# Kernel tuning notes

Hardware: AMD Instinct MI355X
Metric: run time of the kernel (lower is better)

Reference implementation:

```python
import jax, jax.numpy as jnp
import numpy as np

B, S, H, M, E = 8, 2048, 2048, 256, 8
Hh = H // 2

def setup_inputs() -> dict:
    key = jax.random.key(0)
    ks = jax.random.split(key, 12)
    s = 0.02
    return {
        "x":   jax.random.normal(ks[0], (B, S, H), dtype=jnp.float32),
        # metacognitive (router) network: H -> M -> M -> E, softmax
        "Wm1": jax.random.normal(ks[1], (H, M), dtype=jnp.float32) * s,
        "bm1": jnp.zeros((M,), dtype=jnp.float32),
        "Wm2": jax.random.normal(ks[2], (M, M), dtype=jnp.float32) * s,
        "bm2": jnp.zeros((M,), dtype=jnp.float32),
        "Wm3": jax.random.normal(ks[3], (M, E), dtype=jnp.float32) * s,
        "bm3": jnp.zeros((E,), dtype=jnp.float32),
        # stacked expert MLPs: Linear(H,H/2)-ReLU-Linear(H/2,H)-Tanh
        "W1":  jax.random.normal(ks[4], (E, H, Hh), dtype=jnp.float32) * s,
        "b1":  jnp.zeros((E, Hh), dtype=jnp.float32),
        "W2":  jax.random.normal(ks[5], (E, Hh, H), dtype=jnp.float32) * s,
        "b2":  jnp.zeros((E, H), dtype=jnp.float32),
        # strategy_effectiveness buffer (init: ones)
        "eff": jnp.ones((E,), dtype=jnp.float32),
    }

def reference(x, Wm1, bm1, Wm2, bm2, Wm3, bm3, W1, b1, W2, b2, eff):
    # --- select_strategy ---
    pooled = x.mean(axis=1)                                   # [B,H]
    h = jax.nn.relu(pooled @ Wm1 + bm1)                       # [B,M]
    h = jax.nn.relu(h @ Wm2 + bm2)                            # [B,M]
    probs = jax.nn.softmax(h @ Wm3 + bm3, axis=-1)            # [B,E]
    w = jax.nn.softmax(probs * eff[None, :], axis=-1)         # [B,E]
    # --- apply_strategies (all experts batched) ---
    he = jax.nn.relu(jnp.einsum('bsh,ehf->bsef', x, W1) + b1) # [B,S,E,Hh]
    ye = jnp.tanh(jnp.einsum('bsef,efh->bseh', he, W2) + b2)  # [B,S,E,H]
    out = jnp.einsum('bseh,be->bsh', ye, w)                   # [B,S,H]
    return out
```

## Files before the change

kernel.cpp:

```cpp
#include <hip/hip_runtime.h>
#include <hip/hip_bf16.h>
#include <cstdint>
#include <cstddef>

#define B_   8
#define S_   2048
#define H_   2048
#define M_   256
#define E_   8
#define HH_  1024
#define BS_  (B_*S_)

typedef _Float16 f16;
typedef _Float16 f16x8 __attribute__((ext_vector_type(8)));
typedef float    f32x4 __attribute__((ext_vector_type(4)));

#define SLOT_B   49152
#define A_HALF_B 16384
#define B_OFF    32768
#define B_HALF_B 8192

__device__ __forceinline__ void gl_lds16(const void* g, void* l) {
  __builtin_amdgcn_global_load_lds(
      (const __attribute__((address_space(1))) uint32_t*)g,
      (__attribute__((address_space(3))) uint32_t*)l, 16, 0, 0);
}

__device__ __forceinline__ int sinv(int P) {
  int b8 = (P >> 8) & 1, b7 = (P >> 7) & 1, b6 = (P >> 6) & 1;
  return P ^ (b8 << 6) ^ (b7 << 5) ^ ((b6 ^ b8) << 4);
}

__device__ __forceinline__ float fast_tanh(float x) {
  x = fminf(fmaxf(x, -15.f), 15.f);
  float t = __expf(2.f * x);
  return (t - 1.f) / (t + 1.f);
}

template<int NG, int NT_LG, int ASEG_SH, int BSEG_SH, class F>
__device__ __forceinline__ void kloop(const char* aS0, const char* aS1,
    const char* bS0, char* ldsc, int aRd, int bRd, int wv, int ln,
    f32x4 (&acc)[4][4], F fold) {
  constexpr int NT = 1 << NT_LG;

  auto stage = [&](int gs, int ss, int h) {
    int tt = gs & (NT - 1);
    size_t ea = 0, eb = 0;
    if constexpr (ASEG_SH != 0) {
      int e = gs >> NT_LG;
      ea = (size_t)e << ASEG_SH;
      eb = (size_t)e << BSEG_SH;
    }
    int koff = tt * 128 + h * 64;
    char* dA = ldsc + ss * SLOT_B + h * A_HALF_B + wv * 1024 + ln * 16;
    gl_lds16(aS0 + ea + koff, dA);
    gl_lds16(aS1 + ea + koff, dA + 8192);
    char* dB = ldsc + ss * SLOT_B + B_OFF + h * B_HALF_B + wv * 1024 + ln * 16;
    gl_lds16(bS0 + eb + koff, dB);
  };

#pragma unroll
  for (int t = 0; t < 2; ++t) { stage(t, t, 0); stage(t, t, 1); }
  asm volatile("s_waitcnt vmcnt(6)" ::: "memory");
  __builtin_amdgcn_s_barrier();

  int s = 0;
#pragma unroll 1
  for (int g = 0; g < NG; ++g) {
    int ss = s + 2; if (ss >= 3) ss -= 3;
    const char* sbase = ldsc + s * SLOT_B;
    bool do_stage = (g + 2) < NG;
#pragma unroll
    for (int h = 0; h < 2; ++h) {
      f16x8 af[4], bf[4];
      const char* aB = sbase + h * A_HALF_B + aRd;
      const char* bB = sbase + B_OFF + h * B_HALF_B + bRd;
#pragma unroll
      for (int m = 0; m < 4; ++m) af[m] = *(const f16x8*)(aB + m * 1024);
#pragma unroll
      for (int n = 0; n < 4; ++n) bf[n] = *(const f16x8*)(bB + n * 1024);
      if (do_stage) stage(g + 2, ss, h);
      __builtin_amdgcn_sched_barrier(0);
      __builtin_amdgcn_s_barrier();
      asm volatile("s_waitcnt lgkmcnt(0)" ::: "memory");
      __builtin_amdgcn_sched_barrier(0);
      __builtin_amdgcn_s_setprio(1);
#pragma unroll
      for (int m = 0; m < 4; ++m)
#pragma unroll
        for (int n = 0; n < 4; ++n)
          acc[m][n] = __builtin_amdgcn_mfma_f32_16x16x32_f16(af[m], bf[n], acc[m][n], 0, 0, 0);
      __builtin_amdgcn_s_setprio(0);
      __builtin_amdgcn_sched_barrier(0);
      if (h == 1) {
        if ((g & (NT - 1)) == (NT - 1)) fold(g >> NT_LG);
        if (g < NG - 2) { asm volatile("s_waitcnt vmcnt(6)" ::: "memory"); }
        else            { asm volatile("s_waitcnt vmcnt(0)" ::: "memory"); }
        __builtin_amdgcn_sched_barrier(0);
      }
      __builtin_amdgcn_s_barrier();
    }
    ++s; if (s >= 3) s -= 3;
  }
}

__global__ __launch_bounds__(512, 2) void gemm1_pipe(
    const f16* __restrict__ xf, const f16* __restrict__ W1t,
    const float* __restrict__ b1, f16* __restrict__ he) {
  __shared__ f16 lds[3 * 24576];
  char* ldsc = (char*)lds;
  int tid = threadIdx.x, wv = tid >> 6, ln = tid & 63, l15 = ln & 15, kq = ln >> 4;
  int wr = wv >> 1, wc = wv & 1;

  int id = blockIdx.x;
  int logical = (id & 7) * 512 + (id >> 3);
  int nt = logical & 7, mt = (logical >> 3) & 63, e = logical >> 9;
  int brow = mt * 256, bcol = nt * 128;

  int mask = (ln & 7) << 4;
  int aRd = ((wr * 64 + l15) * 64 + kq * 16) ^ mask;
  int bRd = ((wc * 64 + l15) * 64 + kq * 16) ^ mask;

  int PA0 = wv * 1024 + ln * 16;
  int LA0 = sinv(PA0), LA1 = sinv(PA0 + 8192), LB = sinv(PA0);
  const char* aS0 = (const char*)xf + (size_t)(brow + (LA0 >> 6)) * (H_ * 2) + (LA0 & 63);
  const char* aS1 = (const char*)xf + (size_t)(brow + (LA1 >> 6)) * (H_ * 2) + (LA1 & 63);
  const char* bS0 = (const char*)W1t + ((size_t)e * HH_ + bcol + (LB >> 6)) * (H_ * 2) + (LB & 63);

  f32x4 acc[4][4] = {};
  kloop<32, 5, 0, 0>(aS0, aS1, bS0, ldsc, aRd, bRd, wv, ln, acc, [](int) {});

  f16* C = he + (size_t)e * BS_ * HH_;
#pragma unroll
  for (int n = 0; n < 4; ++n) {
    int gc = bcol + wc * 64 + n * 16 + l15;
    float bias = b1[e * HH_ + gc];
#pragma unroll
    for (int m = 0; m < 4; ++m) {
      int gr0 = brow + wr * 64 + m * 16 + kq * 4;
#pragma unroll
      for (int r = 0; r < 4; ++r)
        C[(size_t)(gr0 + r) * HH_ + gc] = (f16)fmaxf(acc[m][n][r] + bias, 0.f);
    }
  }
}

__global__ __launch_bounds__(512, 2) void gemm2_pipe(
    const f16* __restrict__ he, const f16* __restrict__ W2t,
    const float* __restrict__ b2, const float* __restrict__ wbuf,
    float* __restrict__ out) {
  __shared__ f16 lds[3 * 24576];
  char* ldsc = (char*)lds;
  int tid = threadIdx.x, wv = tid >> 6, ln = tid & 63, l15 = ln & 15, kq = ln >> 4;
  int wr = wv >> 1, wc = wv & 1;

  int id = blockIdx.x;
  int logical = (id & 7) * 128 + (id >> 3);
  int nt = logical & 15, mt = logical >> 4;
  int brow = mt * 256, bcol = nt * 128;
  int bb = brow >> 11;

  int mask = (ln & 7) << 4;
  int aRd = ((wr * 64 + l15) * 64 + kq * 16) ^ mask;
  int bRd = ((wc * 64 + l15) * 64 + kq * 16) ^ mask;

  int PA0 = wv * 1024 + ln * 16;
  int LA0 = sinv(PA0), LA1 = sinv(PA0 + 8192), LB = sinv(PA0);
  const char* aS0 = (const char*)he + (size_t)(brow + (LA0 >> 6)) * (HH_ * 2) + (LA0 & 63);
  const char* aS1 = (const char*)he + (size_t)(brow + (LA1 >> 6)) * (HH_ * 2) + (LA1 & 63);
  const char* bS0 = (const char*)W2t + (size_t)(bcol + (LB >> 6)) * (HH_ * 2) + (LB & 63);

  f32x4 acc[4][4] = {};
  f32x4 tot[4][4] = {};

  auto fold = [&](int e) {
    float we = wbuf[bb * E_ + e];
#pragma unroll
    for (int n = 0; n < 4; ++n) {
      float bias = b2[e * H_ + bcol + wc * 64 + n * 16 + l15];
#pragma unroll
      for (int m = 0; m < 4; ++m) {
#pragma unroll
        for (int r = 0; r < 4; ++r) {
          tot[m][n][r] += we * fast_tanh(acc[m][n][r] + bias);
          acc[m][n][r] = 0.f;
        }
      }
    }
  };

  kloop<128, 4, 25, 22>(aS0, aS1, bS0, ldsc, aRd, bRd, wv, ln, acc, fold);

#pragma unroll
  for (int n = 0; n < 4; ++n) {
    int gc = bcol + wc * 64 + n * 16 + l15;
#pragma unroll
    for (int m = 0; m < 4; ++m) {
      int gr0 = brow + wr * 64 + m * 16 + kq * 4;
#pragma unroll
      for (int r = 0; r < 4; ++r)
        out[(size_t)(gr0 + r) * H_ + gc] = tot[m][n][r];
    }
  }
}

__global__ void convert_x_pool(const float* __restrict__ x, f16* __restrict__ xf,
                               float* __restrict__ partial) {
  int h  = blockIdx.x * 256 + threadIdx.x;
  int sc = blockIdx.y;
  int b  = blockIdx.z;
  size_t base = ((size_t)b * S_ + sc * 64) * H_ + h;
  float sum = 0.f;
#pragma unroll 4
  for (int i = 0; i < 64; ++i) {
    float v = x[base + (size_t)i * H_];
    sum += v;
    xf[base + (size_t)i * H_] = (f16)v;
  }
  partial[((size_t)b * H_ + h) * 32 + sc] = sum;
}

__global__ void pool_finalize(const float* __restrict__ partial, float* __restrict__ pooled) {
  int i = blockIdx.x * 256 + threadIdx.x;
  float s = 0.f;
#pragma unroll
  for (int c = 0; c < 32; ++c) s += partial[(size_t)i * 32 + c];
  pooled[i] = s * (1.0f / S_);
}

__global__ void router_kernel(const float* __restrict__ pooled,
                              const float* __restrict__ Wm1, const float* __restrict__ bm1,
                              const float* __restrict__ Wm2, const float* __restrict__ bm2,
                              const float* __restrict__ Wm3, const float* __restrict__ bm3,
                              const float* __restrict__ eff, float* __restrict__ wout) {
  __shared__ float pl[H_];
  __shared__ float h1[M_];
  __shared__ float h2[M_];
  __shared__ float lg[E_];
  int b = blockIdx.x;
  int t = threadIdx.x;

  for (int i = t; i < H_; i += 256) pl[i] = pooled[b * H_ + i];
  __syncthreads();

  float s = bm1[t];
  for (int k = 0; k < H_; ++k) s += pl[k] * Wm1[(size_t)k * M_ + t];
  h1[t] = fmaxf(s, 0.f);
  __syncthreads();

  s = bm2[t];
  for (int k = 0; k < M_; ++k) s += h1[k] * Wm2[k * M_ + t];
  h2[t] = fmaxf(s, 0.f);
  __syncthreads();

  if (t < E_) {
    float l = bm3[t];
    for (int k = 0; k < M_; ++k) l += h2[k] * Wm3[k * E_ + t];
    lg[t] = l;
  }
  __syncthreads();

  if (t == 0) {
    float p[E_], q[E_];
    float mx = -1e30f;
    for (int e = 0; e < E_; ++e) mx = fmaxf(mx, lg[e]);
    float den = 0.f;
    for (int e = 0; e < E_; ++e) { p[e] = __expf(lg[e] - mx); den += p[e]; }
    float inv = 1.f / den;
    for (int e = 0; e < E_; ++e) q[e] = p[e] * inv * eff[e];
    mx = -1e30f;
    for (int e = 0; e < E_; ++e) mx = fmaxf(mx, q[e]);
    den = 0.f;
    for (int e = 0; e < E_; ++e) { q[e] = __expf(q[e] - mx); den += q[e]; }
    inv = 1.f / den;
    for (int e = 0; e < E_; ++e) wout[b * E_ + e] = q[e] * inv;
  }
}

__global__ void transpose_cvt(const float* __restrict__ in, f16* __restrict__ out,
                              int R, int C) {
  __shared__ f16 tile[32][33];
  int e  = blockIdx.z;
  int c0 = blockIdx.x * 32, r0 = blockIdx.y * 32;
  int tx = threadIdx.x & 31, ty = threadIdx.x >> 5;
  const float* inp = in + (size_t)e * R * C;
  f16* outp = out + (size_t)e * R * C;
#pragma unroll
  for (int i = 0; i < 4; ++i) {
    int r = r0 + ty + i * 8;
    tile[ty + i * 8][tx] = (f16)inp[(size_t)r * C + c0 + tx];
  }
  __syncthreads();
#pragma unroll
  for (int i = 0; i < 4; ++i) {
    int c = c0 + ty + i * 8;
    outp[(size_t)c * R + r0 + tx] = tile[tx][ty + i * 8];
  }
}

extern "C" void kernel_launch(void* const* d_in, const int* in_sizes, int n_in,
                              void* d_out, int out_size, void* d_ws, size_t ws_size,
                              hipStream_t stream) {
  const float* x   = (const float*)d_in[0];
  const float* Wm1 = (const float*)d_in[1];
  const float* bm1 = (const float*)d_in[2];
  const float* Wm2 = (const float*)d_in[3];
  const float* bm2 = (const float*)d_in[4];
  const float* Wm3 = (const float*)d_in[5];
  const float* bm3 = (const float*)d_in[6];
  const float* W1  = (const float*)d_in[7];
  const float* b1  = (const float*)d_in[8];
  const float* W2  = (const float*)d_in[9];
  const float* b2  = (const float*)d_in[10];
  const float* eff = (const float*)d_in[11];
  float* out = (float*)d_out;

  char* ws = (char*)d_ws;
  size_t off = 0;
  auto take = [&](size_t bytes) { void* p = ws + off; off += (bytes + 255) & ~(size_t)255; return p; };

  f16*   xf      = (f16*)  take((size_t)BS_ * H_ * 2);
  f16*   W1t     = (f16*)  take((size_t)E_ * HH_ * H_ * 2);
  f16*   W2t     = (f16*)  take((size_t)E_ * H_ * HH_ * 2);
  float* partial = (float*)take((size_t)B_ * H_ * 32 * 4);
  float* pooled  = (float*)take((size_t)B_ * H_ * 4);
  float* wbuf    = (float*)take(1024);
  f16*   he      = (f16*)  take((size_t)E_ * BS_ * HH_ * 2);

  convert_x_pool<<<dim3(H_ / 256, S_ / 64, B_), 256, 0, stream>>>(x, xf, partial);
  pool_finalize<<<(B_ * H_) / 256, 256, 0, stream>>>(partial, pooled);
  router_kernel<<<B_, 256, 0, stream>>>(pooled, Wm1, bm1, Wm2, bm2, Wm3, bm3, eff, wbuf);
  transpose_cvt<<<dim3(HH_ / 32, H_ / 32, E_), 256, 0, stream>>>(W1, W1t, H_, HH_);
  transpose_cvt<<<dim3(H_ / 32, HH_ / 32, E_), 256, 0, stream>>>(W2, W2t, HH_, H_);

  gemm1_pipe<<<4096, 512, 0, stream>>>(xf, W1t, b1, he);
  gemm2_pipe<<<1024, 512, 0, stream>>>(he, W2t, b2, wbuf, out);
}
```

Before: 1.623 ms.

## Merge k-loop halves into one barrier per stage; cache gemm2 bias in LDS

The pipelined k-loop now reads both K-halves of A and B fragments up front, issues both async stage loads together, and runs all 32 MFMAs back to back. This replaces the two s_barrier/lgkmcnt synchronisations per stage with a single end-of-iteration barrier, cutting synchronisation stalls. In gemm2, the per-expert b2 bias slice and the routing weights are preloaded into shared memory once, so the fold step no longer does scattered global loads. The cost is doubled fragment registers, which may raise VGPR pressure or cause spills under the 512-thread launch bound, and less interleaving of LDS reads with MFMAs.

```diff
diff --git a/kernel.cpp b/kernel.cpp
--- a/kernel.cpp
+++ b/kernel.cpp
@@ -69,37 +69,37 @@
   for (int g = 0; g < NG; ++g) {
     int ss = s + 2; if (ss >= 3) ss -= 3;
     const char* sbase = ldsc + s * SLOT_B;
-    bool do_stage = (g + 2) < NG;
+    __builtin_amdgcn_sched_barrier(0);
+
+    f16x8 af[2][4], bf[2][4];
 #pragma unroll
     for (int h = 0; h < 2; ++h) {
-      f16x8 af[4], bf[4];
       const char* aB = sbase + h * A_HALF_B + aRd;
       const char* bB = sbase + B_OFF + h * B_HALF_B + bRd;
 #pragma unroll
-      for (int m = 0; m < 4; ++m) af[m] = *(const f16x8*)(aB + m * 1024);
-#pragma unroll
-      for (int n = 0; n < 4; ++n) bf[n] = *(const f16x8*)(bB + n * 1024);
-      if (do_stage) stage(g + 2, ss, h);
-      __builtin_amdgcn_sched_barrier(0);
-      __builtin_amdgcn_s_barrier();
-      asm volatile("s_waitcnt lgkmcnt(0)" ::: "memory");
-      __builtin_amdgcn_sched_barrier(0);
-      __builtin_amdgcn_s_setprio(1);
+      for (int m = 0; m < 4; ++m) af[h][m] = *(const f16x8*)(aB + m * 1024);
+#pragma unroll
+      for (int n = 0; n < 4; ++n) bf[h][n] = *(const f16x8*)(bB + n * 1024);
+    }
+
+    if ((g + 2) < NG) { stage(g + 2, ss, 0); stage(g + 2, ss, 1); }
+
+    __builtin_amdgcn_s_setprio(1);
+#pragma unroll
+    for (int h = 0; h < 2; ++h)
 #pragma unroll
       for (int m = 0; m < 4; ++m)
 #pragma unroll
         for (int n = 0; n < 4; ++n)
-          acc[m][n] = __builtin_amdgcn_mfma_f32_16x16x32_f16(af[m], bf[n], acc[m][n], 0, 0, 0);
-      __builtin_amdgcn_s_setprio(0);
-      __builtin_amdgcn_sched_barrier(0);
-      if (h == 1) {
-        if ((g & (NT - 1)) == (NT - 1)) fold(g >> NT_LG);
-        if (g < NG - 2) { asm volatile("s_waitcnt vmcnt(6)" ::: "memory"); }
-        else            { asm volatile("s_waitcnt vmcnt(0)" ::: "memory"); }
-        __builtin_amdgcn_sched_barrier(0);
-      }
-      __builtin_amdgcn_s_barrier();
-    }
+          acc[m][n] = __builtin_amdgcn_mfma_f32_16x16x32_f16(af[h][m], bf[h][n], acc[m][n], 0, 0, 0);
+    __builtin_amdgcn_s_setprio(0);
+
+    if ((g & (NT - 1)) == (NT - 1)) fold(g >> NT_LG);
+
+    __builtin_amdgcn_sched_barrier(0);
+    if (g < NG - 2) { asm volatile("s_waitcnt vmcnt(6)" ::: "memory"); }
+    else            { asm volatile("s_waitcnt vmcnt(0)" ::: "memory"); }
+    __builtin_amdgcn_s_barrier();
     ++s; if (s >= 3) s -= 3;
   }
 }
@@ -150,6 +150,8 @@
     const float* __restrict__ b2, const float* __restrict__ wbuf,
     float* __restrict__ out) {
   __shared__ f16 lds[3 * 24576];
+  __shared__ float biasLDS[E_][128];
+  __shared__ float wLDS[E_];
   char* ldsc = (char*)lds;
   int tid = threadIdx.x, wv = tid >> 6, ln = tid & 63, l15 = ln & 15, kq = ln >> 4;
   int wr = wv >> 1, wc = wv & 1;
@@ -160,6 +162,17 @@
   int brow = mt * 256, bcol = nt * 128;
   int bb = brow >> 11;
 
+  {
+    int i = tid;
+#pragma unroll
+    for (int rep = 0; rep < 2; ++rep, i += 512) {
+      int e = i >> 7, c = i & 127;
+      biasLDS[e][c] = b2[e * H_ + bcol + c];
+    }
+    if (tid < E_) wLDS[tid] = wbuf[bb * E_ + tid];
+  }
+  __syncthreads();
+
   int mask = (ln & 7) << 4;
   int aRd = ((wr * 64 + l15) * 64 + kq * 16) ^ mask;
   int bRd = ((wc * 64 + l15) * 64 + kq * 16) ^ mask;
@@ -174,10 +187,10 @@
   f32x4 tot[4][4] = {};
 
   auto fold = [&](int e) {
-    float we = wbuf[bb * E_ + e];
+    float we = wLDS[e];
 #pragma unroll
     for (int n = 0; n < 4; ++n) {
-      float bias = b2[e * H_ + bcol + wc * 64 + n * 16 + l15];
+      float bias = biasLDS[e][wc * 64 + n * 16 + l15];
 #pragma unroll
       for (int m = 0; m < 4; ++m) {
 #pragma unroll
```

New measurement: 1.483 ms. 8.6% less time.
